# Performance work log

Hardware: AMD Instinct MI355X
Metric: run time of the kernel (lower is better)

The kernel has to match this reference:

```python
import jax, jax.numpy as jnp
import numpy as np

B, C, H, W = 8, 256, 200, 200
D_IN, D_HID, D_OUT = 256, 1024, 40000

def setup_inputs() -> dict:
    key = jax.random.key(0)
    k1, k2, k3, k4, k5, k6 = jax.random.split(key, 6)
    x = jax.random.normal(k1, (B, C, H, W), dtype=jnp.float32)
    localization = jax.random.normal(k2, (B, D_IN), dtype=jnp.float32)
    # Linear params (PyTorch default init scale ~ 1/sqrt(fan_in))
    W1 = jax.random.normal(k3, (D_IN, D_HID), dtype=jnp.float32) / np.sqrt(D_IN)
    b1 = jax.random.normal(k4, (D_HID,), dtype=jnp.float32) / np.sqrt(D_IN)
    W2 = jax.random.normal(k5, (D_HID, D_OUT), dtype=jnp.float32) / np.sqrt(D_HID)
    b2 = jax.random.normal(k6, (D_OUT,), dtype=jnp.float32) / np.sqrt(D_HID)
    return {"x": x, "localization": localization, "W1": W1, "b1": b1, "W2": W2, "b2": b2}

def reference(x, localization, W1, b1, W2, b2):
    # MLP: Linear(256,1024) -> LeakyReLU(0.1) -> Linear(1024,40000)
    h = localization @ W1 + b1
    h = jnp.where(h >= 0, h, 0.1 * h)
    w = h @ W2 + b2                      # [B, 40000]
    w = w.reshape(x.shape[0], 200, 200)  # [B, 200, 200]
    # Vectorized form of the nested loop: x[i,j] += x[i,j] * w[i]
    return x * (1.0 + w[:, None, :, :])
```

## Files before the change

kernel.cpp:

```cpp
#include <hip/hip_runtime.h>

#define B_    8
#define D_IN  256
#define D_HID 1024
#define D_OUT 40000
#define HW4   10000
#define CHW4  2560000
#define TOT4  20480000

typedef float f32x4 __attribute__((ext_vector_type(4)));

__global__ void mlp1_kernel(const float* __restrict__ loc,
                            const float* __restrict__ W1,
                            const float* __restrict__ b1,
                            float* __restrict__ hT) {
    __shared__ float red[256];
    int g    = blockIdx.x;
    int b    = g >> 4;
    int k0   = (g & 15) * 64;
    int w    = threadIdx.x >> 6;
    int lane = threadIdx.x & 63;
    int k    = k0 + lane;

    float acc = 0.0f;
    #pragma unroll 8
    for (int ii = 0; ii < 64; ++ii) {
        int i = w * 64 + ii;
        acc += loc[b * D_IN + i] * W1[i * D_HID + k];
    }
    red[threadIdx.x] = acc;
    __syncthreads();
    if (w == 0) {
        float s = red[lane] + red[64 + lane] + red[128 + lane] + red[192 + lane];
        s += b1[k];
        s = (s >= 0.0f) ? s : 0.1f * s;
        hT[k * B_ + b] = s;
    }
}

template<int KS>
__global__ void mlp2_partial_kernel(const float* __restrict__ hT,
                                    const float* __restrict__ W2,
                                    float* __restrict__ partial) {
    constexpr int CHUNK = D_HID / KS;
    int j4 = blockIdx.x * 64 + threadIdx.x;
    if (j4 >= HW4) return;
    int ks = blockIdx.y;
    int k0 = ks * CHUNK;
    const f32x4* __restrict__ W24 = (const f32x4*)W2;
    f32x4 acc[B_];
    #pragma unroll
    for (int b = 0; b < B_; ++b) acc[b] = (f32x4)0.0f;
    #pragma unroll 8
    for (int kk = 0; kk < CHUNK; ++kk) {
        int k = k0 + kk;
        f32x4 wv = __builtin_nontemporal_load(&W24[k * HW4 + j4]);
        const float* __restrict__ h = &hT[k * B_];
        #pragma unroll
        for (int b = 0; b < B_; ++b)
            acc[b] += wv * h[b];
    }
    f32x4* __restrict__ p4 = (f32x4*)partial;
    #pragma unroll
    for (int b = 0; b < B_; ++b)
        __builtin_nontemporal_store(acc[b], &p4[(ks * B_ + b) * HW4 + j4]);
}

template<int KS>
__global__ void mlp2_reduce_kernel(const float* __restrict__ partial,
                                   const float* __restrict__ b2,
                                   float* __restrict__ wmap) {
    int t = blockIdx.x * blockDim.x + threadIdx.x;
    if (t >= B_ * HW4) return;
    int b = t / HW4;
    int j4 = t - b * HW4;
    const f32x4* __restrict__ p4  = (const f32x4*)partial;
    const f32x4* __restrict__ b24 = (const f32x4*)b2;
    f32x4 s = b24[j4] + 1.0f;
    #pragma unroll
    for (int ks = 0; ks < KS; ++ks)
        s += __builtin_nontemporal_load(&p4[(ks * B_ + b) * HW4 + j4]);
    ((f32x4*)wmap)[b * HW4 + j4] = s;
}

__global__ void scale_kernel(const float* __restrict__ x,
                             const float* __restrict__ wmap,
                             float* __restrict__ out) {
    const f32x4* __restrict__ x4 = (const f32x4*)x;
    const f32x4* __restrict__ w4 = (const f32x4*)wmap;
    f32x4* __restrict__ o4 = (f32x4*)out;
    int stride = gridDim.x * blockDim.x;
    for (int i = blockIdx.x * blockDim.x + threadIdx.x; i < TOT4; i += stride) {
        unsigned int b  = (unsigned int)i / CHW4;
        unsigned int p4 = (unsigned int)i % HW4;
        f32x4 xv = __builtin_nontemporal_load(&x4[i]);
        f32x4 wv = w4[b * HW4 + p4];
        __builtin_nontemporal_store(xv * wv, &o4[i]);
    }
}

template<int KS>
static void launch_mlp2(const float* hT, const float* W2, const float* b2,
                        float* partial, float* wmap, hipStream_t stream) {
    dim3 g2(157, KS);
    mlp2_partial_kernel<KS><<<g2, 64, 0, stream>>>(hT, W2, partial);
    mlp2_reduce_kernel<KS><<<(B_ * HW4 + 255) / 256, 256, 0, stream>>>(partial, b2, wmap);
}

extern "C" void kernel_launch(void* const* d_in, const int* in_sizes, int n_in,
                              void* d_out, int out_size, void* d_ws, size_t ws_size,
                              hipStream_t stream) {
    const float* x   = (const float*)d_in[0];
    const float* loc = (const float*)d_in[1];
    const float* W1  = (const float*)d_in[2];
    const float* b1  = (const float*)d_in[3];
    const float* W2  = (const float*)d_in[4];
    const float* b2  = (const float*)d_in[5];
    float* out = (float*)d_out;

    float* hT      = (float*)d_ws;
    float* partial = (float*)((char*)d_ws + 32768);

    size_t base = 32768;
    int KS = 1;
    for (int cand = 16; cand >= 1; cand >>= 1) {
        size_t need = base + (size_t)(cand + 1) * B_ * D_OUT * sizeof(float);
        if (need <= ws_size) { KS = cand; break; }
    }
    float* wmap = (float*)((char*)d_ws + base
                           + (size_t)KS * B_ * D_OUT * sizeof(float));

    mlp1_kernel<<<128, 256, 0, stream>>>(loc, W1, b1, hT);

    switch (KS) {
        case 16: launch_mlp2<16>(hT, W2, b2, partial, wmap, stream); break;
        case 8:  launch_mlp2<8> (hT, W2, b2, partial, wmap, stream); break;
        case 4:  launch_mlp2<4> (hT, W2, b2, partial, wmap, stream); break;
        case 2:  launch_mlp2<2> (hT, W2, b2, partial, wmap, stream); break;
        default: launch_mlp2<1> (hT, W2, b2, partial, wmap, stream); break;
    }

    scale_kernel<<<2048, 256, 0, stream>>>(x, wmap, out);
}
```

Before: 164.9 us.

## Fuse MLP, reduction and scaling into one persistent kernel with grid barriers

Replaces the four separate launches with one persistent kernel of 512 blocks. The kernel runs the first linear layer, the split-K second layer, the partial reduction and the broadcast scaling in phases, separated by a software grid barrier built on atomics. The second-layer units are handed out dynamically through an atomic work counter, with one wave per unit. This removes the launch gaps and tail effects between kernels. In exchange it adds barrier spin costs and needs a memset of the barrier state each call. It also relies on all 512 blocks being co-resident, and the scaling phase now runs with fewer threads than the old 2048-block launch.

```diff
diff --git a/kernel.cpp b/kernel.cpp
--- a/kernel.cpp
+++ b/kernel.cpp
@@ -7,104 +7,156 @@
 #define HW4   10000
 #define CHW4  2560000
 #define TOT4  20480000
+#define NBLK  512
+#define NTHR  256
 
 typedef float f32x4 __attribute__((ext_vector_type(4)));
+typedef unsigned long long u64;
 
-__global__ void mlp1_kernel(const float* __restrict__ loc,
-                            const float* __restrict__ W1,
-                            const float* __restrict__ b1,
-                            float* __restrict__ hT) {
-    __shared__ float red[256];
-    int g    = blockIdx.x;
-    int b    = g >> 4;
-    int k0   = (g & 15) * 64;
-    int w    = threadIdx.x >> 6;
-    int lane = threadIdx.x & 63;
-    int k    = k0 + lane;
+__device__ __forceinline__ void grid_barrier(unsigned* cnt, unsigned* gen) {
+    __syncthreads();
+    if (threadIdx.x == 0) {
+        unsigned g = __hip_atomic_load(gen, __ATOMIC_RELAXED, __HIP_MEMORY_SCOPE_AGENT);
+        unsigned prev = __hip_atomic_fetch_add(cnt, 1u, __ATOMIC_ACQ_REL, __HIP_MEMORY_SCOPE_AGENT);
+        if (prev == (unsigned)(NBLK - 1)) {
+            __hip_atomic_store(cnt, 0u, __ATOMIC_RELAXED, __HIP_MEMORY_SCOPE_AGENT);
+            __hip_atomic_store(gen, g + 1u, __ATOMIC_RELEASE, __HIP_MEMORY_SCOPE_AGENT);
+        } else {
+            while (__hip_atomic_load(gen, __ATOMIC_RELAXED, __HIP_MEMORY_SCOPE_AGENT) == g)
+                __builtin_amdgcn_s_sleep(16);
+            __builtin_amdgcn_fence(__ATOMIC_ACQUIRE, "agent");
+        }
+    }
+    __syncthreads();
+}
 
-    float acc = 0.0f;
-    #pragma unroll 8
-    for (int ii = 0; ii < 64; ++ii) {
-        int i = w * 64 + ii;
-        acc += loc[b * D_IN + i] * W1[i * D_HID + k];
+__device__ __forceinline__ void store16_agent(f32x4 v, f32x4* p) {
+    union { f32x4 v; u64 q[2]; } u;
+    u.v = v;
+    u64* d = (u64*)p;
+    __hip_atomic_store(d,     u.q[0], __ATOMIC_RELAXED, __HIP_MEMORY_SCOPE_AGENT);
+    __hip_atomic_store(d + 1, u.q[1], __ATOMIC_RELAXED, __HIP_MEMORY_SCOPE_AGENT);
+}
+
+template<int KS>
+__global__ __launch_bounds__(NTHR, 4)
+void fused_kernel(const float* __restrict__ x,
+                  const float* __restrict__ loc,
+                  const float* __restrict__ W1,
+                  const float* __restrict__ b1,
+                  const float* __restrict__ W2,
+                  const float* __restrict__ b2,
+                  float* __restrict__ out,
+                  unsigned* __restrict__ bar,
+                  float* __restrict__ hT,
+                  float* __restrict__ partial,
+                  float* __restrict__ wmap) {
+    unsigned* cnt  = bar;
+    unsigned* gen  = bar + 32;
+    unsigned* work = bar + 64;
+
+    __shared__ float red[NTHR];
+    const int bid  = blockIdx.x;
+    const int tid  = threadIdx.x;
+    const int wid  = tid >> 6;
+    const int lane = tid & 63;
+
+    if (bid < 128) {
+        int b  = bid >> 4;
+        int k0 = (bid & 15) * 64;
+        int k  = k0 + lane;
+        float acc = 0.0f;
+        #pragma unroll 8
+        for (int ii = 0; ii < 64; ++ii) {
+            int i = wid * 64 + ii;
+            acc += loc[b * D_IN + i] * W1[i * D_HID + k];
+        }
+        red[tid] = acc;
+        __syncthreads();
+        if (wid == 0) {
+            float s = red[lane] + red[64 + lane] + red[128 + lane] + red[192 + lane];
+            s += b1[k];
+            s = (s >= 0.0f) ? s : 0.1f * s;
+            __hip_atomic_store(&hT[k * B_ + b], s, __ATOMIC_RELAXED, __HIP_MEMORY_SCOPE_AGENT);
+        }
     }
-    red[threadIdx.x] = acc;
-    __syncthreads();
-    if (w == 0) {
-        float s = red[lane] + red[64 + lane] + red[128 + lane] + red[192 + lane];
-        s += b1[k];
-        s = (s >= 0.0f) ? s : 0.1f * s;
-        hT[k * B_ + b] = s;
+    grid_barrier(cnt, gen);
+
+    {
+        constexpr int CHUNK  = D_HID / KS;
+        constexpr unsigned NUNITS = 157u * KS;
+        const f32x4* __restrict__ W24 = (const f32x4*)W2;
+        f32x4* __restrict__ p4 = (f32x4*)partial;
+        for (;;) {
+            unsigned u;
+            if (lane == 0)
+                u = __hip_atomic_fetch_add(work, 1u, __ATOMIC_RELAXED, __HIP_MEMORY_SCOPE_AGENT);
+            u = (unsigned)__shfl((int)u, 0);
+            if (u >= NUNITS) break;
+            int jblk = (int)(u % 157u);
+            int ks   = (int)(u / 157u);
+            int j4   = jblk * 64 + lane;
+            if (j4 < HW4) {
+                int k0 = ks * CHUNK;
+                f32x4 acc[B_];
+                #pragma unroll
+                for (int b = 0; b < B_; ++b) acc[b] = (f32x4)0.0f;
+                #pragma unroll 4
+                for (int kk = 0; kk < CHUNK; ++kk) {
+                    int k = k0 + kk;
+                    f32x4 wv = __builtin_nontemporal_load(&W24[k * HW4 + j4]);
+                    const float* __restrict__ h = &hT[k * B_];
+                    #pragma unroll
+                    for (int b = 0; b < B_; ++b)
+                        acc[b] += wv * h[b];
+                }
+                #pragma unroll
+                for (int b = 0; b < B_; ++b)
+                    store16_agent(acc[b], &p4[(ks * B_ + b) * HW4 + j4]);
+            }
+        }
+    }
+    grid_barrier(cnt, gen);
+
+    {
+        int t = bid * NTHR + tid;
+        if (t < B_ * HW4) {
+            int b  = t / HW4;
+            int j4 = t - b * HW4;
+            const f32x4* __restrict__ p4  = (const f32x4*)partial;
+            const f32x4* __restrict__ b24 = (const f32x4*)b2;
+            f32x4 s = b24[j4] + 1.0f;
+            #pragma unroll
+            for (int ks = 0; ks < KS; ++ks)
+                s += p4[(ks * B_ + b) * HW4 + j4];
+            store16_agent(s, &((f32x4*)wmap)[b * HW4 + j4]);
+        }
+    }
+    grid_barrier(cnt, gen);
+
+    {
+        const f32x4* __restrict__ x4 = (const f32x4*)x;
+        const f32x4* __restrict__ w4 = (const f32x4*)wmap;
+        f32x4* __restrict__ o4 = (f32x4*)out;
+        const int stride = NBLK * NTHR;
+        #pragma unroll 4
+        for (int i = bid * NTHR + tid; i < TOT4; i += stride) {
+            unsigned int b = (unsigned int)i / CHW4;
+            unsigned int p = (unsigned int)i % HW4;
+            f32x4 xv = __builtin_nontemporal_load(&x4[i]);
+            f32x4 wv = w4[b * HW4 + p];
+            __builtin_nontemporal_store(xv * wv, &o4[i]);
+        }
     }
 }
 
 template<int KS>
-__global__ void mlp2_partial_kernel(const float* __restrict__ hT,
-                                    const float* __restrict__ W2,
-                                    float* __restrict__ partial) {
-    constexpr int CHUNK = D_HID / KS;
-    int j4 = blockIdx.x * 64 + threadIdx.x;
-    if (j4 >= HW4) return;
-    int ks = blockIdx.y;
-    int k0 = ks * CHUNK;
-    const f32x4* __restrict__ W24 = (const f32x4*)W2;
-    f32x4 acc[B_];
-    #pragma unroll
-    for (int b = 0; b < B_; ++b) acc[b] = (f32x4)0.0f;
-    #pragma unroll 8
-    for (int kk = 0; kk < CHUNK; ++kk) {
-        int k = k0 + kk;
-        f32x4 wv = __builtin_nontemporal_load(&W24[k * HW4 + j4]);
-        const float* __restrict__ h = &hT[k * B_];
-        #pragma unroll
-        for (int b = 0; b < B_; ++b)
-            acc[b] += wv * h[b];
-    }
-    f32x4* __restrict__ p4 = (f32x4*)partial;
-    #pragma unroll
-    for (int b = 0; b < B_; ++b)
-        __builtin_nontemporal_store(acc[b], &p4[(ks * B_ + b) * HW4 + j4]);
-}
-
-template<int KS>
-__global__ void mlp2_reduce_kernel(const float* __restrict__ partial,
-                                   const float* __restrict__ b2,
-                                   float* __restrict__ wmap) {
-    int t = blockIdx.x * blockDim.x + threadIdx.x;
-    if (t >= B_ * HW4) return;
-    int b = t / HW4;
-    int j4 = t - b * HW4;
-    const f32x4* __restrict__ p4  = (const f32x4*)partial;
-    const f32x4* __restrict__ b24 = (const f32x4*)b2;
-    f32x4 s = b24[j4] + 1.0f;
-    #pragma unroll
-    for (int ks = 0; ks < KS; ++ks)
-        s += __builtin_nontemporal_load(&p4[(ks * B_ + b) * HW4 + j4]);
-    ((f32x4*)wmap)[b * HW4 + j4] = s;
-}
-
-__global__ void scale_kernel(const float* __restrict__ x,
-                             const float* __restrict__ wmap,
-                             float* __restrict__ out) {
-    const f32x4* __restrict__ x4 = (const f32x4*)x;
-    const f32x4* __restrict__ w4 = (const f32x4*)wmap;
-    f32x4* __restrict__ o4 = (f32x4*)out;
-    int stride = gridDim.x * blockDim.x;
-    for (int i = blockIdx.x * blockDim.x + threadIdx.x; i < TOT4; i += stride) {
-        unsigned int b  = (unsigned int)i / CHW4;
-        unsigned int p4 = (unsigned int)i % HW4;
-        f32x4 xv = __builtin_nontemporal_load(&x4[i]);
-        f32x4 wv = w4[b * HW4 + p4];
-        __builtin_nontemporal_store(xv * wv, &o4[i]);
-    }
-}
-
-template<int KS>
-static void launch_mlp2(const float* hT, const float* W2, const float* b2,
-                        float* partial, float* wmap, hipStream_t stream) {
-    dim3 g2(157, KS);
-    mlp2_partial_kernel<KS><<<g2, 64, 0, stream>>>(hT, W2, partial);
-    mlp2_reduce_kernel<KS><<<(B_ * HW4 + 255) / 256, 256, 0, stream>>>(partial, b2, wmap);
+static void launch_fused(const float* x, const float* loc, const float* W1,
+                         const float* b1, const float* W2, const float* b2,
+                         float* out, unsigned* bar, float* hT, float* partial,
+                         float* wmap, hipStream_t stream) {
+    fused_kernel<KS><<<NBLK, NTHR, 0, stream>>>(x, loc, W1, b1, W2, b2, out,
+                                                bar, hT, partial, wmap);
 }
 
 extern "C" void kernel_launch(void* const* d_in, const int* in_sizes, int n_in,
@@ -118,10 +170,11 @@
     const float* b2  = (const float*)d_in[5];
     float* out = (float*)d_out;
 
-    float* hT      = (float*)d_ws;
-    float* partial = (float*)((char*)d_ws + 32768);
+    unsigned* bar  = (unsigned*)d_ws;
+    float* hT      = (float*)((char*)d_ws + 512);
+    float* partial = (float*)((char*)d_ws + 512 + 32768);
 
-    size_t base = 32768;
+    size_t base = 512 + 32768;
     int KS = 1;
     for (int cand = 16; cand >= 1; cand >>= 1) {
         size_t need = base + (size_t)(cand + 1) * B_ * D_OUT * sizeof(float);
@@ -130,15 +183,13 @@
     float* wmap = (float*)((char*)d_ws + base
                            + (size_t)KS * B_ * D_OUT * sizeof(float));
 
-    mlp1_kernel<<<128, 256, 0, stream>>>(loc, W1, b1, hT);
+    hipMemsetAsync(d_ws, 0, 512, stream);
 
     switch (KS) {
-        case 16: launch_mlp2<16>(hT, W2, b2, partial, wmap, stream); break;
-        case 8:  launch_mlp2<8> (hT, W2, b2, partial, wmap, stream); break;
-        case 4:  launch_mlp2<4> (hT, W2, b2, partial, wmap, stream); break;
-        case 2:  launch_mlp2<2> (hT, W2, b2, partial, wmap, stream); break;
-        default: launch_mlp2<1> (hT, W2, b2, partial, wmap, stream); break;
+        case 16: launch_fused<16>(x, loc, W1, b1, W2, b2, out, bar, hT, partial, wmap, stream); break;
+        case 8:  launch_fused<8> (x, loc, W1, b1, W2, b2, out, bar, hT, partial, wmap, stream); break;
+        case 4:  launch_fused<4> (x, loc, W1, b1, W2, b2, out, bar, hT, partial, wmap, stream); break;
+        case 2:  launch_fused<2> (x, loc, W1, b1, W2, b2, out, bar, hT, partial, wmap, stream); break;
+        default: launch_fused<1> (x, loc, W1, b1, W2, b2, out, bar, hT, partial, wmap, stream); break;
     }
-
-    scale_kernel<<<2048, 256, 0, stream>>>(x, wmap, out);
 }
```

Result: slower. 269.7 us (+63.5%).
